# Kernel tuning notes

Hardware: AMD Instinct MI355X
Metric: run time of the kernel (lower is better)

The kernel has to match this reference:

```python
import jax, jax.numpy as jnp
import numpy as np

N = 256
IL_MMI = 0.02      # insertion loss MMI
IMB = 0.01         # imbalance MMI
IL_CR = 0.02       # insertion loss Crossing
CT = 0.01          # cross talk Crossing


def _mmi_matrix():
    # 2x2 MMI: sqrt(1-IL)*[[t, i r],[i r, t]] with t=sqrt((1+imb)/2), r=sqrt((1-imb)/2)
    a = np.sqrt(1.0 - IL_MMI)
    t = np.sqrt((1.0 + IMB) / 2.0)
    r = np.sqrt((1.0 - IMB) / 2.0)
    mmi2 = a * np.array([[t, 1j * r], [1j * r, t]], dtype=np.complex64)
    # block-diagonal over even pairs (0,1),(2,3),...
    return jnp.asarray(np.kron(np.eye(N // 2, dtype=np.complex64), mmi2))


def _crossing_matrix():
    # pairs start at odd index 1; rows 0 and N-1 pass through with amplitude sqrt(1-IL)*sqrt(1-CT)
    a = np.sqrt(1.0 - IL_CR)
    thru = a * np.sqrt(1.0 - CT)
    cr2 = a * np.array([[np.sqrt(CT), 1j * np.sqrt(1.0 - CT)],
                        [1j * np.sqrt(1.0 - CT), np.sqrt(CT)]], dtype=np.complex64)
    M = np.zeros((N, N), dtype=np.complex64)
    M[0, 0] = thru
    for i in range(1, N - 1, 2):
        M[i:i + 2, i:i + 2] = cr2
    if N % 2 == 0:
        M[-1, -1] = thru
    return jnp.asarray(M)


def setup_inputs() -> dict:
    key = jax.random.key(0)
    thetas = jax.random.uniform(key, (N // 2 + 2, N), dtype=jnp.float32) * (2.0 * np.pi)
    return {"thetas": thetas}


def reference(thetas):
    MMI = _mmi_matrix()
    CR = _crossing_matrix()
    phases = jnp.exp(1j * thetas)  # [N//2+2, N] complex64; diag phase-shift layers

    # arch = ht[0] @ I  (diagonal left-multiply == row scaling)
    arch0 = jnp.diag(phases[0])

    def body(arch, ph):
        # one mesh stage with trailing crossing (iterations i = 0 .. N//2-2)
        arch = MMI @ arch
        arch = ph[:, None] * arch      # ht[i+1] @ arch
        arch = MMI @ arch
        arch = CR @ arch
        return arch, None

    arch, _ = jax.lax.scan(body, arch0, phases[1:N // 2])

    # last loop iteration (i = N//2-1): no crossing
    arch = MMI @ arch
    arch = phases[N // 2][:, None] * arch
    arch = MMI @ arch
    # final phase layer ht[N//2+1]
    arch = phases[N // 2 + 1][:, None] * arch
    return arch
```

## Files before the change

### kernel.cpp

```cpp
#include <hip/hip_runtime.h>


__device__ __forceinline__ float dpp_up1(float x) {
    return __int_as_float(__builtin_amdgcn_update_dpp(
        __float_as_int(x), __float_as_int(x), 0x138, 0xf, 0xf, false));
}
__device__ __forceinline__ float dpp_dn1(float x) {
    return __int_as_float(__builtin_amdgcn_update_dpp(
        __float_as_int(x), __float_as_int(x), 0x130, 0xf, 0xf, false));
}
__device__ __forceinline__ void sincos4(float4 th, float sn[4], float cs[4]) {
    __sincosf(th.x, &sn[0], &cs[0]);
    __sincosf(th.y, &sn[1], &cs[1]);
    __sincosf(th.z, &sn[2], &cs[2]);
    __sincosf(th.w, &sn[3], &cs[3]);
}

__device__ __forceinline__ float2 cmul_pk(float2 K, float2 z) {
    float2 t;
    asm("v_pk_mul_f32 %0, %1, %2 op_sel:[0,0] op_sel_hi:[0,1]\n\t"
        "v_pk_fma_f32 %0, %1, %2, %0 op_sel:[1,1,0] op_sel_hi:[1,0,1] neg_lo:[1,0,0]"
        : "=&v"(t) : "v"(K), "v"(z));
    return t;
}
__device__ __forceinline__ float2 cfma_pk(float2 K, float2 z, float2 acc) {
    asm("v_pk_fma_f32 %0, %1, %2, %0 op_sel:[0,0,0] op_sel_hi:[0,1,1]\n\t"
        "v_pk_fma_f32 %0, %1, %2, %0 op_sel:[1,1,0] op_sel_hi:[1,0,1] neg_lo:[1,0,0]"
        : "+v"(acc) : "v"(K), "v"(z));
    return acc;
}
__device__ __forceinline__ float2 cross_pk(float2 K, float2 z, float2 p) {
    float2 t;
    asm("v_pk_mul_f32 %0, %1, %2 op_sel:[0,0] op_sel_hi:[0,1]\n\t"
        "v_pk_fma_f32 %0, %1, %3, %0 op_sel:[1,1,0] op_sel_hi:[1,0,1] neg_lo:[1,0,0]"
        : "=&v"(t) : "v"(K), "v"(z), "v"(p));
    return t;
}

__global__ __launch_bounds__(64)
void coef_kernel(const float* __restrict__ thetas,
                 float* __restrict__ coefs)
{
    const int s0   = blockIdx.x;
    const int lane = threadIdx.x;

    const float U  = 0.98f * 0.505f;
    const float W  = 0.98f * 0.495f;
    const float Gc = 0.98f * sqrtf(0.505f * 0.495f);

    float4 th = *(const float4*)(thetas + (s0 + 1) * 256 + 4 * lane);
    float s[4], c[4];
    sincos4(th, s, c);

    float4 A, B, C;
    A.x = U * c[0] - W * c[1];   A.y = U * s[0] - W * s[1];
    A.z = U * c[1] - W * c[0];   A.w = U * s[1] - W * s[0];
    B.x = -Gc * (s[0] + s[1]);   B.y = Gc * (c[0] + c[1]);
    B.z = -Gc * (s[2] + s[3]);   B.w = Gc * (c[2] + c[3]);
    C.x = U * c[2] - W * c[3];   C.y = U * s[2] - W * s[3];
    C.z = U * c[3] - W * c[2];   C.w = U * s[3] - W * s[2];

    float4* cp = (float4*)coefs;
    cp[(s0 * 3 + 0) * 64 + lane] = A;
    cp[(s0 * 3 + 1) * 64 + lane] = B;
    cp[(s0 * 3 + 2) * 64 + lane] = C;
}

__global__ __launch_bounds__(64, 1)
void neuropuls_mesh_kernel(const float* __restrict__ thetas,
                           const float* __restrict__ coefs,
                           float* __restrict__ out)
{
    constexpr int N = 256;
    __shared__ float4 cbuf[2][1536];

    const int lane = threadIdx.x;
    const int col  = blockIdx.x;

    const float BT = sqrtf(0.98f * 0.01f);
    const float BR = sqrtf(0.98f * 0.99f);
    const float2 CK  = make_float2(BT, BR);
    const float2 EC0 = (lane == 0)  ? make_float2(BR, 0.f) : CK;
    const float2 EC3 = (lane == 63) ? make_float2(BR, 0.f) : CK;

    float2 z0 = make_float2(0.f, 0.f), z1 = z0, z2 = z0, z3 = z0;

    {
        const float th0 = thetas[col];
        float s0, c0;
        __sincosf(th0, &s0, &c0);
        const int r0 = col - 4 * lane;
        if (r0 == 0) z0 = make_float2(c0, s0);
        else if (r0 == 1) z1 = make_float2(c0, s0);
        else if (r0 == 2) z2 = make_float2(c0, s0);
        else if (r0 == 3) z3 = make_float2(c0, s0);
    }

    auto mstep = [&](const float4& KA, const float4& KB, const float4& KC) {
        const float2 E0 = make_float2(KA.x, KA.y), F0 = make_float2(KA.z, KA.w);
        const float2 G0 = make_float2(KB.x, KB.y), G1 = make_float2(KB.z, KB.w);
        const float2 E1 = make_float2(KC.x, KC.y), F1 = make_float2(KC.z, KC.w);
        const float2 nx0 = cfma_pk(G0, z1, cmul_pk(E0, z0));
        const float2 ny0 = cfma_pk(F0, z1, cmul_pk(G0, z0));
        const float2 nx1 = cfma_pk(G1, z3, cmul_pk(E1, z2));
        const float2 ny1 = cfma_pk(F1, z3, cmul_pk(G1, z2));
        z0 = nx0; z1 = ny0; z2 = nx1; z3 = ny1;
    };
    auto crossing = [&]() {
        const float2 pv3 = make_float2(dpp_up1(z3.x), dpp_up1(z3.y));
        const float2 nv0 = make_float2(dpp_dn1(z0.x), dpp_dn1(z0.y));
        const float2 t1 = cross_pk(CK, z1, z2);
        const float2 t2 = cross_pk(CK, z2, z1);
        z0 = cross_pk(EC0, z0, pv3);
        z3 = cross_pk(EC3, z3, nv0);
        z1 = t1; z2 = t2;
    };

    auto issue_chunk = [&](int c) {
        const float4* src = (const float4*)coefs + (c * 24) * 64 + lane;
        float4* dst = &cbuf[c & 1][0];
        #pragma unroll
        for (int j = 0; j < 24; ++j)
            __builtin_amdgcn_global_load_lds(
                (const __attribute__((address_space(1))) void*)(src + j * 64),
                (__attribute__((address_space(3))) void*)(dst + j * 64),
                16, 0, 0);
    };

    issue_chunk(0);
    issue_chunk(1);
    asm volatile("s_waitcnt vmcnt(24)" ::: "memory");
    __builtin_amdgcn_sched_barrier(0);

    for (int c = 0; c < 15; ++c) {
        const int cb = c & 1;
        float4 KA[8], KB[8], KC[8];
        #pragma unroll
        for (int k = 0; k < 8; ++k) {
            const float4* p = &cbuf[cb][k * 192 + lane];
            KA[k] = p[0]; KB[k] = p[64]; KC[k] = p[128];
        }
        asm volatile("s_waitcnt lgkmcnt(0)" ::: "memory");
        __builtin_amdgcn_sched_barrier(0);
        if (c <= 13) issue_chunk(c + 2);
        #pragma unroll
        for (int k = 0; k < 8; ++k) {
            mstep(KA[k], KB[k], KC[k]);
            crossing();
        }
        if (c <= 13)
            asm volatile("s_waitcnt vmcnt(24)" ::: "memory");
        else
            asm volatile("s_waitcnt vmcnt(0)" ::: "memory");
        __builtin_amdgcn_sched_barrier(0);
    }

    {
        float4 KA[8], KB[8], KC[8];
        #pragma unroll
        for (int k = 0; k < 8; ++k) {
            const float4* p = &cbuf[1][k * 192 + lane];
            KA[k] = p[0]; KB[k] = p[64]; KC[k] = p[128];
        }
        asm volatile("s_waitcnt lgkmcnt(0)" ::: "memory");
        __builtin_amdgcn_sched_barrier(0);
        #pragma unroll
        for (int k = 0; k < 7; ++k) {
            mstep(KA[k], KB[k], KC[k]);
            crossing();
        }
        mstep(KA[7], KB[7], KC[7]);
    }

    {
        float4 thF = *(const float4*)(thetas + 129 * N + 4 * lane);
        float sn[4], cs[4];
        sincos4(thF, sn, cs);
        z0 = cmul_pk(make_float2(cs[0], sn[0]), z0);
        z1 = cmul_pk(make_float2(cs[1], sn[1]), z1);
        z2 = cmul_pk(make_float2(cs[2], sn[2]), z2);
        z3 = cmul_pk(make_float2(cs[3], sn[3]), z3);
    }

    {
        const int r = 4 * lane;
        out[(r + 0) * N + col] = z0.x;  out[N * N + (r + 0) * N + col] = z0.y;
        out[(r + 1) * N + col] = z1.x;  out[N * N + (r + 1) * N + col] = z1.y;
        out[(r + 2) * N + col] = z2.x;  out[N * N + (r + 2) * N + col] = z2.y;
        out[(r + 3) * N + col] = z3.x;  out[N * N + (r + 3) * N + col] = z3.y;
    }
}

extern "C" void kernel_launch(void* const* d_in, const int* in_sizes, int n_in,
                              void* d_out, int out_size, void* d_ws, size_t ws_size,
                              hipStream_t stream)
{
    const float* thetas = (const float*)d_in[0];
    float* out   = (float*)d_out;
    float* coefs = (float*)d_ws;
    (void)in_sizes; (void)n_in; (void)out_size; (void)ws_size;

    coef_kernel<<<dim3(128), dim3(64), 0, stream>>>(thetas, coefs);
    neuropuls_mesh_kernel<<<dim3(256), dim3(64), 0, stream>>>(thetas, coefs, out);
}
```

Baseline: 71.46 us.

## Split mesh stages into two parallel halves and combine with a complex matmul

The 128-stage sequential mesh is split into two independent halves of 64 stages each. Each half runs as its own set of 256 column blocks (512 blocks total) and writes an intermediate 256x256 complex matrix to workspace. A new combine kernel then multiplies the two halves together with a naive complex matrix product. This halves the serial dependency chain and doubles the number of blocks on the device, at the cost of an extra kernel launch, workspace traffic and a 256^3 complex matmul.

```diff
diff --git a/kernel.cpp b/kernel.cpp
--- a/kernel.cpp
+++ b/kernel.cpp
@@ -67,15 +67,17 @@
 }
 
 __global__ __launch_bounds__(64, 1)
-void neuropuls_mesh_kernel(const float* __restrict__ thetas,
-                           const float* __restrict__ coefs,
-                           float* __restrict__ out)
+void group_kernel(const float* __restrict__ thetas,
+                  const float* __restrict__ coefs,
+                  float* __restrict__ ws)
 {
     constexpr int N = 256;
     __shared__ float4 cbuf[2][1536];
 
+    const int g    = blockIdx.x >> 8;
+    const int col  = blockIdx.x & 255;
     const int lane = threadIdx.x;
-    const int col  = blockIdx.x;
+    const int base = g * 8;
 
     const float BT = sqrtf(0.98f * 0.01f);
     const float BR = sqrtf(0.98f * 0.99f);
@@ -86,14 +88,17 @@
     float2 z0 = make_float2(0.f, 0.f), z1 = z0, z2 = z0, z3 = z0;
 
     {
-        const float th0 = thetas[col];
-        float s0, c0;
-        __sincosf(th0, &s0, &c0);
         const int r0 = col - 4 * lane;
-        if (r0 == 0) z0 = make_float2(c0, s0);
-        else if (r0 == 1) z1 = make_float2(c0, s0);
-        else if (r0 == 2) z2 = make_float2(c0, s0);
-        else if (r0 == 3) z3 = make_float2(c0, s0);
+        if (0 <= r0 && r0 < 4) {
+            float2 v = make_float2(1.f, 0.f);
+            if (g == 0) {
+                float s0, c0;
+                __sincosf(thetas[col], &s0, &c0);
+                v = make_float2(c0, s0);
+            }
+            if (r0 == 0) z0 = v; else if (r0 == 1) z1 = v;
+            else if (r0 == 2) z2 = v; else z3 = v;
+        }
     }
 
     auto mstep = [&](const float4& KA, const float4& KB, const float4& KC) {
@@ -117,7 +122,7 @@
     };
 
     auto issue_chunk = [&](int c) {
-        const float4* src = (const float4*)coefs + (c * 24) * 64 + lane;
+        const float4* src = (const float4*)coefs + ((base + c) * 24) * 64 + lane;
         float4* dst = &cbuf[c & 1][0];
         #pragma unroll
         for (int j = 0; j < 24; ++j)
@@ -132,7 +137,7 @@
     asm volatile("s_waitcnt vmcnt(24)" ::: "memory");
     __builtin_amdgcn_sched_barrier(0);
 
-    for (int c = 0; c < 15; ++c) {
+    for (int c = 0; c < 7; ++c) {
         const int cb = c & 1;
         float4 KA[8], KB[8], KC[8];
         #pragma unroll
@@ -142,13 +147,13 @@
         }
         asm volatile("s_waitcnt lgkmcnt(0)" ::: "memory");
         __builtin_amdgcn_sched_barrier(0);
-        if (c <= 13) issue_chunk(c + 2);
+        if (c <= 5) issue_chunk(c + 2);
         #pragma unroll
         for (int k = 0; k < 8; ++k) {
             mstep(KA[k], KB[k], KC[k]);
             crossing();
         }
-        if (c <= 13)
+        if (c <= 5)
             asm volatile("s_waitcnt vmcnt(24)" ::: "memory");
         else
             asm volatile("s_waitcnt vmcnt(0)" ::: "memory");
@@ -170,9 +175,10 @@
             crossing();
         }
         mstep(KA[7], KB[7], KC[7]);
-    }
-
-    {
+        if (g == 0) crossing();
+    }
+
+    if (g == 1) {
         float4 thF = *(const float4*)(thetas + 129 * N + 4 * lane);
         float sn[4], cs[4];
         sincos4(thF, sn, cs);
@@ -183,12 +189,45 @@
     }
 
     {
+        float2* pb = (float2*)(ws + (g == 0 ? 98304 : 229376));
         const int r = 4 * lane;
-        out[(r + 0) * N + col] = z0.x;  out[N * N + (r + 0) * N + col] = z0.y;
-        out[(r + 1) * N + col] = z1.x;  out[N * N + (r + 1) * N + col] = z1.y;
-        out[(r + 2) * N + col] = z2.x;  out[N * N + (r + 2) * N + col] = z2.y;
-        out[(r + 3) * N + col] = z3.x;  out[N * N + (r + 3) * N + col] = z3.y;
-    }
+        pb[(r + 0) * 256 + col] = z0;
+        pb[(r + 1) * 256 + col] = z1;
+        pb[(r + 2) * 256 + col] = z2;
+        pb[(r + 3) * 256 + col] = z3;
+    }
+}
+
+__global__ __launch_bounds__(256)
+void combine_kernel(const float* __restrict__ ws,
+                    float* __restrict__ out)
+{
+    const int c  = threadIdx.x;
+    const int r0 = blockIdx.x * 2;
+
+    const float2* A = (const float2*)(ws + 229376);
+    const float2* B = (const float2*)(ws + 98304);
+    const float2* a0p = A + (size_t)r0 * 256;
+    const float2* a1p = A + (size_t)(r0 + 1) * 256;
+    const float2* bp  = B + c;
+
+    float ar0 = 0.f, ai0 = 0.f, ar1 = 0.f, ai1 = 0.f;
+    #pragma unroll 8
+    for (int k = 0; k < 256; ++k) {
+        const float2 a0 = a0p[k];
+        const float2 a1 = a1p[k];
+        const float2 b  = bp[(size_t)k * 256];
+        ar0 += a0.x * b.x - a0.y * b.y;
+        ai0 += a0.x * b.y + a0.y * b.x;
+        ar1 += a1.x * b.x - a1.y * b.y;
+        ai1 += a1.x * b.y + a1.y * b.x;
+    }
+
+    const int i0 = r0 * 256 + c;
+    out[i0]               = ar0;
+    out[65536 + i0]       = ai0;
+    out[i0 + 256]         = ar1;
+    out[65536 + i0 + 256] = ai1;
 }
 
 extern "C" void kernel_launch(void* const* d_in, const int* in_sizes, int n_in,
@@ -196,10 +235,11 @@
                               hipStream_t stream)
 {
     const float* thetas = (const float*)d_in[0];
-    float* out   = (float*)d_out;
-    float* coefs = (float*)d_ws;
+    float* out = (float*)d_out;
+    float* ws  = (float*)d_ws;
     (void)in_sizes; (void)n_in; (void)out_size; (void)ws_size;
 
-    coef_kernel<<<dim3(128), dim3(64), 0, stream>>>(thetas, coefs);
-    neuropuls_mesh_kernel<<<dim3(256), dim3(64), 0, stream>>>(thetas, coefs, out);
-}
+    coef_kernel   <<<dim3(128), dim3(64),  0, stream>>>(thetas, ws);
+    group_kernel  <<<dim3(512), dim3(64),  0, stream>>>(thetas, ws, ws);
+    combine_kernel<<<dim3(128), dim3(256), 0, stream>>>(ws, out);
+}
```

Result: slower. 81.92 us (+14.6%).
